# Optimization experiments

Hardware: AMD Instinct MI355X
Metric: run time of the kernel (lower is better)

## Reference

```python
import jax, jax.numpy as jnp
import numpy as np

D_MODEL = 1024
D_STATE = 64
D_CONV = 4
EXPAND = 2
HEADDIM = 64
D_INNER = EXPAND * D_MODEL            # 2048
NHEADS = D_INNER // HEADDIM           # 32
CONV_DIM = D_INNER + 2 * D_STATE      # 2176
D_IN_PROJ = 2 * D_INNER + 2 * D_STATE + NHEADS  # 4256
B, L = 2, 1024


def _mamba2(x, in_proj_w, conv_w, conv_b, dt_bias, A_log, D_param, rms_w, out_proj_w):
    b, l, _ = x.shape
    zxbcdt = x @ in_proj_w.T                                   # (b,l,4256)
    z, xBC, dt = jnp.split(zxbcdt, [D_INNER, D_INNER + CONV_DIM], axis=-1)
    dt = jax.nn.softplus(dt + dt_bias)                         # (b,l,h)
    # depthwise causal conv over sequence
    xBC = jax.lax.conv_general_dilated(
        xBC, conv_w, (1,), [(D_CONV - 1, 0)],
        dimension_numbers=("NLC", "LIO", "NLC"),
        feature_group_count=CONV_DIM) + conv_b
    xBC = jax.nn.silu(xBC)
    xs, Bmat, Cmat = jnp.split(xBC, [D_INNER, D_INNER + D_STATE], axis=-1)
    xh = xs.reshape(b, l, NHEADS, HEADDIM)
    A = -jnp.exp(A_log)                                        # (h,)
    dA = jnp.exp(dt * A)                                       # (b,l,h)

    def step(h, inp):
        dA_t, dt_t, B_t, C_t, x_t = inp                        # (b,h),(b,h),(b,n),(b,n),(b,h,p)
        h = h * dA_t[..., None, None] + (dt_t[..., None] * x_t)[..., None] * B_t[:, None, None, :]
        y_t = jnp.einsum("bhpn,bn->bhp", h, C_t)
        return h, y_t

    h0 = jnp.zeros((b, NHEADS, HEADDIM, D_STATE), x.dtype)
    inps = (dA.transpose(1, 0, 2), dt.transpose(1, 0, 2),
            Bmat.transpose(1, 0, 2), Cmat.transpose(1, 0, 2),
            xh.transpose(1, 0, 2, 3))
    _, ys = jax.lax.scan(step, h0, inps)                       # (l,b,h,p)
    y = ys.transpose(1, 0, 2, 3) + D_param[None, None, :, None] * xh
    y = y.reshape(b, l, D_INNER)
    # gated RMSNorm (norm after gating, as in mamba_ssm RMSNormGated)
    y = y * jax.nn.silu(z)
    y = y * jax.lax.rsqrt(jnp.mean(y * y, axis=-1, keepdims=True) + 1e-5) * rms_w
    return y @ out_proj_w.T


def setup_inputs() -> dict:
    key = jax.random.key(0)
    ks = jax.random.split(key, 16)
    s = 0.02

    def mamba_params(i):
        kk = jax.random.split(ks[i], 8)
        dt = jnp.exp(jax.random.uniform(kk[4], (NHEADS,)) * (np.log(0.1) - np.log(1e-3)) + np.log(1e-3))
        dt_bias = dt + jnp.log(-jnp.expm1(-dt))
        return dict(
            in_proj_w=jax.random.normal(kk[0], (D_IN_PROJ, D_MODEL)) * s,
            conv_w=jax.random.normal(kk[1], (D_CONV, 1, CONV_DIM)) * 0.2,
            conv_b=jnp.zeros((CONV_DIM,)),
            dt_bias=dt_bias,
            A_log=jnp.log(jax.random.uniform(kk[2], (NHEADS,), minval=1.0, maxval=16.0)),
            D=jnp.ones((NHEADS,)),
            rms_w=jnp.ones((D_INNER,)),
            out_proj_w=jax.random.normal(kk[3], (D_MODEL, D_INNER)) * s,
        )

    pf = mamba_params(1)
    pb = mamba_params(2)
    inp = {"x": jax.random.normal(ks[0], (B, L, D_MODEL))}
    for name, v in pf.items():
        inp["f_" + name] = v
    for name, v in pb.items():
        inp["b_" + name] = v
    inp["proj_w"] = jax.random.normal(ks[3], (D_MODEL, 2 * D_MODEL)) * s
    inp["proj_b"] = jnp.zeros((D_MODEL,))
    inp["ln_w"] = jnp.ones((D_MODEL,))
    inp["ln_b"] = jnp.zeros((D_MODEL,))
    return inp


def reference(x, f_in_proj_w, f_conv_w, f_conv_b, f_dt_bias, f_A_log, f_D, f_rms_w, f_out_proj_w,
              b_in_proj_w, b_conv_w, b_conv_b, b_dt_bias, b_A_log, b_D, b_rms_w, b_out_proj_w,
              proj_w, proj_b, ln_w, ln_b):
    out_fwd = _mamba2(x, f_in_proj_w, f_conv_w, f_conv_b, f_dt_bias, f_A_log, f_D, f_rms_w, f_out_proj_w)
    out_bwd = _mamba2(jnp.flip(x, 1), b_in_proj_w, b_conv_w, b_conv_b, b_dt_bias, b_A_log, b_D, b_rms_w, b_out_proj_w)
    out_bwd = jnp.flip(out_bwd, 1)
    combined = jnp.concatenate([out_fwd, out_bwd], axis=-1)
    h = x + combined @ proj_w.T + proj_b
    mu = jnp.mean(h, axis=-1, keepdims=True)
    var = jnp.mean((h - mu) ** 2, axis=-1, keepdims=True)
    return (h - mu) * jax.lax.rsqrt(var + 1e-5) * ln_w + ln_b
```

## Files before the change

### kernel.cpp

```cpp
#include <hip/hip_runtime.h>
#include <hip/hip_bf16.h>

#define DEV __device__ __forceinline__

typedef short bf16x8 __attribute__((ext_vector_type(8)));
typedef float f32x4 __attribute__((ext_vector_type(4)));

static constexpr int BATCH  = 2;
static constexpr int SEQ    = 1024;
static constexpr int DMODEL = 1024;
static constexpr int DINNER = 2048;
static constexpr int DSTATE = 64;
static constexpr int NH     = 32;
static constexpr int HD     = 64;
static constexpr int CONVD  = 2176;
static constexpr int DPROJ  = 4256;
static constexpr int MROWS  = BATCH * SEQ;
static constexpr int NCHUNK = 16;
static constexpr int QC     = 64;

static constexpr size_t OFF_ZX = 0;
static constexpr size_t OFF_XS = OFF_ZX + (size_t)2*MROWS*DPROJ*2;
static constexpr size_t OFF_BB = OFF_XS + (size_t)2*MROWS*DINNER*2;
static constexpr size_t OFF_CC = OFF_BB + (size_t)2*MROWS*DSTATE*4;
static constexpr size_t OFF_DT = OFF_CC + (size_t)2*MROWS*DSTATE*4;
static constexpr size_t OFF_DA = OFF_DT + (size_t)2*MROWS*NH*4;
static constexpr size_t OFF_DR = OFF_DA + (size_t)2*MROWS*NH*4;
static constexpr size_t OFF_CS = OFF_DR + (size_t)2*MROWS*NH*4;
static constexpr size_t OFF_DD = 0;
static constexpr size_t OFF_H  = OFF_DD + (size_t)MROWS*2*DMODEL;
static constexpr size_t OFF_WO = OFF_H  + (size_t)MROWS*DMODEL*4;
static constexpr size_t OFF_WP = OFF_WO + (size_t)2*DMODEL*DINNER*2;

DEV float b2f(ushort u) {
    union { unsigned int i; float f; } v;
    v.i = ((unsigned int)u) << 16;
    return v.f;
}
DEV ushort f2b(float f) {
    union { float f; unsigned int u; } v;
    v.f = f;
    unsigned int r = 0x7FFFu + ((v.u >> 16) & 1u);
    return (ushort)((v.u + r) >> 16);
}
DEV bf16x8 pack8(float4 a, float4 b) {
    bf16x8 r;
    r[0] = (short)f2b(a.x); r[1] = (short)f2b(a.y);
    r[2] = (short)f2b(a.z); r[3] = (short)f2b(a.w);
    r[4] = (short)f2b(b.x); r[5] = (short)f2b(b.y);
    r[6] = (short)f2b(b.z); r[7] = (short)f2b(b.w);
    return r;
}
DEV void gll16(const ushort* g, ushort* l) {
    __builtin_amdgcn_global_load_lds(
        (const __attribute__((address_space(1))) unsigned int*)g,
        (__attribute__((address_space(3))) unsigned int*)l, 16, 0, 0);
}

__global__ __launch_bounds__(256) void cvt3_k(
    const float* __restrict__ s0, const float* __restrict__ s1,
    const float* __restrict__ s2,
    ushort* __restrict__ d0, ushort* __restrict__ d1, ushort* __restrict__ d2,
    int b0, int b1)
{
    int blk = blockIdx.x;
    const float* s; ushort* d; size_t off;
    if (blk < b0)            { s = s0; d = d0; off = (size_t)blk * 1024; }
    else if (blk < b0 + b1)  { s = s1; d = d1; off = (size_t)(blk - b0) * 1024; }
    else                     { s = s2; d = d2; off = (size_t)(blk - b0 - b1) * 1024; }
    size_t i = off + threadIdx.x * 4;
    float4 f = *(const float4*)(s + i);
    ushort4 u;
    u.x = f2b(f.x); u.y = f2b(f.y); u.z = f2b(f.z); u.w = f2b(f.w);
    *(ushort4*)(d + i) = u;
}

template<int MODE, int BN>
__global__ __launch_bounds__(256) void gemm_k(
    const ushort* __restrict__ A, const ushort* __restrict__ W,
    size_t wstride, void* __restrict__ outp, const float* __restrict__ resid,
    const float* __restrict__ bias, float* __restrict__ dtraw,
    int N, int K)
{
    constexpr int BM = 128, BK = 64;
    constexpr int MT = (BN == 128) ? 4 : 2;
    constexpr int NBLB = (BN == 128) ? 4 : 2;
    __shared__ ushort As[BM * BK];
    __shared__ ushort Bs[BN * BK];
    const int tid = threadIdx.x;
    const int wave = tid >> 6, lane = tid & 63;
    const int quad = lane >> 4, l16 = lane & 15;
    const int bxu = (MODE == 0)
        ? (int)((blockIdx.x + 2 * blockIdx.y) % gridDim.x) : (int)blockIdx.x;
    const int bn = bxu * BN, bm = blockIdx.y * BM;
    const int dir = blockIdx.z;
    const ushort* Wd = W + (size_t)dir * wstride;
    const int wmoff = (BN == 128) ? (wave >> 1) * 64 : wave * 32;
    const int wnoff = (BN == 128) ? (wave & 1) * 64 : 0;

    const int scg = ((lane & 7) ^ ((lane >> 3) & 7)) * 8;
    const ushort* aga[4];
    ushort* ald[4];
    #pragma unroll
    for (int t = 0; t < 4; t++) {
        int li = wave * 4 + t;
        int r = li * 8 + (lane >> 3);
        int m = bm + r;
        size_t rowidx;
        if (MODE == 0) {
            int b = m >> 10, l = m & 1023;
            int ls = dir ? (1023 - l) : l;
            rowidx = (size_t)((b << 10) + ls);
        } else if (MODE == 1) {
            rowidx = (size_t)(dir * MROWS + m);
        } else {
            rowidx = (size_t)m;
        }
        aga[t] = A + rowidx * K + scg;
        ald[t] = &As[li * 512];
    }
    const ushort* bga[NBLB];
    ushort* bld[NBLB];
    #pragma unroll
    for (int t = 0; t < NBLB; t++) {
        int li = wave * NBLB + t;
        int n = bn + li * 8 + (lane >> 3);
        if (n >= N) n = N - 1;
        bga[t] = Wd + (size_t)n * K + scg;
        bld[t] = &Bs[li * 512];
    }

    f32x4 acc[MT][4] = {};

    for (int k0 = 0; k0 < K; k0 += BK) {
        #pragma unroll
        for (int t = 0; t < 4; t++) gll16(aga[t] + k0, ald[t]);
        #pragma unroll
        for (int t = 0; t < NBLB; t++) gll16(bga[t] + k0, bld[t]);
        __syncthreads();

        #pragma unroll
        for (int kt = 0; kt < 2; kt++) {
            const int rs = (((kt * 4 + quad) ^ (l16 & 7))) * 8;
            bf16x8 af[MT], bfr[4];
            #pragma unroll
            for (int mt = 0; mt < MT; mt++)
                af[mt] = *(const bf16x8*)&As[(wmoff + mt * 16 + l16) * BK + rs];
            #pragma unroll
            for (int nt = 0; nt < 4; nt++)
                bfr[nt] = *(const bf16x8*)&Bs[(wnoff + nt * 16 + l16) * BK + rs];
            #pragma unroll
            for (int mt = 0; mt < MT; mt++)
                #pragma unroll
                for (int nt = 0; nt < 4; nt++)
                    acc[mt][nt] = __builtin_amdgcn_mfma_f32_16x16x32_bf16(
                        af[mt], bfr[nt], acc[mt][nt], 0, 0, 0);
        }
        __syncthreads();
    }

    #pragma unroll
    for (int mt = 0; mt < MT; mt++) {
        #pragma unroll
        for (int nt = 0; nt < 4; nt++) {
            #pragma unroll
            for (int j = 0; j < 4; j++) {
                int row = bm + wmoff + mt * 16 + quad * 4 + j;
                int col = bn + wnoff + nt * 16 + l16;
                if (col >= N) continue;
                float v = acc[mt][nt][j];
                if (MODE == 0) {
                    ((ushort*)outp)[(size_t)(dir * MROWS + row) * DPROJ + col] = f2b(v);
                    if (col >= 4224)
                        dtraw[(size_t)(dir * MROWS + row) * NH + (col - 4224)] = v;
                } else if (MODE == 1) {
                    int mr = dir ? ((row & 1024) | (1023 - (row & 1023))) : row;
                    ((ushort*)outp)[(size_t)mr * (2 * DMODEL) + dir * DMODEL + col] = f2b(v);
                } else {
                    float r = resid[(size_t)row * DMODEL + col] + bias[col];
                    ((float*)outp)[(size_t)row * DMODEL + col] = v + r;
                }
            }
        }
    }
}

__global__ __launch_bounds__(256) void conv_k(
    const ushort* __restrict__ zx, const float* __restrict__ dtr,
    const float* __restrict__ cw0, const float* __restrict__ cb0,
    const float* __restrict__ cw1, const float* __restrict__ cb1,
    const float* __restrict__ dtb0, const float* __restrict__ al0,
    const float* __restrict__ dtb1, const float* __restrict__ al1,
    ushort* __restrict__ xs, float* __restrict__ Bq, float* __restrict__ Cq,
    float* __restrict__ dtq, float* __restrict__ ldq)
{
    int id = blockIdx.x;
    int dir = id >> 11;
    int m = id & 2047;
    int l = m & 1023;
    const float* cw = dir ? cw1 : cw0;
    const float* cb = dir ? cb1 : cb0;
    int tid = threadIdx.x;

    for (int c = tid * 4; c < CONVD; c += 1024) {
        float4 cbv = *(const float4*)&cb[c];
        float acc[4] = { cbv.x, cbv.y, cbv.z, cbv.w };
        #pragma unroll
        for (int t = 0; t < 4; t++) {
            int ls = l - 3 + t;
            if (ls >= 0) {
                float4 wv = *(const float4*)&cw[t * CONVD + c];
                ushort4 xv = *(const ushort4*)&zx[(size_t)(id - l + ls) * DPROJ + 2048 + c];
                acc[0] += wv.x * b2f(xv.x);
                acc[1] += wv.y * b2f(xv.y);
                acc[2] += wv.z * b2f(xv.z);
                acc[3] += wv.w * b2f(xv.w);
            }
        }
        float v[4];
        #pragma unroll
        for (int i = 0; i < 4; i++) v[i] = acc[i] / (1.f + expf(-acc[i]));
        if (c < DINNER) {
            ushort4 u;
            u.x = f2b(v[0]); u.y = f2b(v[1]); u.z = f2b(v[2]); u.w = f2b(v[3]);
            *(ushort4*)&xs[(size_t)id * DINNER + c] = u;
        } else if (c < DINNER + DSTATE) {
            *(float4*)&Bq[(size_t)id * DSTATE + (c - DINNER)] =
                make_float4(v[0], v[1], v[2], v[3]);
        } else {
            *(float4*)&Cq[(size_t)id * DSTATE + (c - DINNER - DSTATE)] =
                make_float4(v[0], v[1], v[2], v[3]);
        }
    }
    if (tid < NH) {
        const float* dtb = dir ? dtb1 : dtb0;
        const float* al  = dir ? al1 : al0;
        float raw = dtr[(size_t)id * NH + tid] + dtb[tid];
        float dt = raw > 20.f ? raw : log1pf(expf(raw));
        float ldA = -expf(al[tid]) * dt;
        int dirb = id >> 10;
        dtq[(size_t)(dirb * NH + tid) * SEQ + l] = dt;
        ldq[(size_t)(dirb * NH + tid) * SEQ + l] = ldA;
    }
}

__global__ __launch_bounds__(256) void states_k(
    const float* __restrict__ Bq, const float* __restrict__ dtT,
    const float* __restrict__ ldT, const ushort* __restrict__ xsq,
    ushort* __restrict__ cs)
{
    int id = blockIdx.x;
    int h = id & 31;
    int c = blockIdx.y;
    int tid = threadIdx.x;
    int wave = tid >> 6, lane = tid & 63;
    int quad = lane >> 4;
    int base = (id >> 5) << 10;
    int l0 = c * QC;

    __shared__ float wsh[QC];
    __shared__ ushort Xw[64][80];
    __shared__ ushort Bt[64][72];

    if (tid < 64) {
        float ld = ldT[(size_t)id * SEQ + l0 + tid];
        #pragma unroll
        for (int st = 1; st < 64; st <<= 1) {
            float o = __shfl_up(ld, st);
            if (tid >= st) ld += o;
        }
        float tot = __shfl(ld, 63);
        wsh[tid] = dtT[(size_t)id * SEQ + l0 + tid] * expf(tot - ld);
    }
    __syncthreads();

    {
        int j = tid >> 2, p0 = (tid & 3) * 16;
        float wj = wsh[j];
        const ushort* xrow = xsq + (size_t)(base + l0 + j) * DINNER + h * HD + p0;
        #pragma unroll
        for (int q = 0; q < 4; q++) {
            ushort4 xv = *(const ushort4*)(xrow + q * 4);
            Xw[p0 + q * 4 + 0][j] = f2b(b2f(xv.x) * wj);
            Xw[p0 + q * 4 + 1][j] = f2b(b2f(xv.y) * wj);
            Xw[p0 + q * 4 + 2][j] = f2b(b2f(xv.z) * wj);
            Xw[p0 + q * 4 + 3][j] = f2b(b2f(xv.w) * wj);
        }
        int j2 = lane, ng = wave * 16;
        const float* brow = Bq + (size_t)(base + l0 + j2) * DSTATE + ng;
        #pragma unroll
        for (int q = 0; q < 4; q++) {
            float4 f = *(const float4*)(brow + q * 4);
            Bt[ng + q * 4 + 0][j2] = f2b(f.x);
            Bt[ng + q * 4 + 1][j2] = f2b(f.y);
            Bt[ng + q * 4 + 2][j2] = f2b(f.z);
            Bt[ng + q * 4 + 3][j2] = f2b(f.w);
        }
    }
    __syncthreads();

    f32x4 acc[4] = {};
    #pragma unroll
    for (int kt = 0; kt < 2; kt++) {
        int k = kt * 32 + quad * 8;
        bf16x8 af = *(const bf16x8*)&Xw[wave * 16 + (lane & 15)][k];
        #pragma unroll
        for (int ni = 0; ni < 4; ni++) {
            bf16x8 bf = *(const bf16x8*)&Bt[ni * 16 + (lane & 15)][k];
            acc[ni] = __builtin_amdgcn_mfma_f32_16x16x32_bf16(af, bf, acc[ni], 0, 0, 0);
        }
    }

    ushort* out = cs + ((size_t)id * NCHUNK + c) * HD * DSTATE;
    #pragma unroll
    for (int ni = 0; ni < 4; ni++) {
        #pragma unroll
        for (int j = 0; j < 4; j++) {
            int p = wave * 16 + quad * 4 + j;
            int n = ni * 16 + (lane & 15);
            out[(size_t)p * DSTATE + n] = f2b(acc[ni][j]);
        }
    }
}

__global__ __launch_bounds__(256) void stitch_k(
    const float* __restrict__ ldT, ushort* __restrict__ cs)
{
    int id = blockIdx.x;
    int tid = threadIdx.x;
    __shared__ float red[256];
    __shared__ float dec[NCHUNK];

    float4 d4 = *(const float4*)(ldT + (size_t)id * SEQ + tid * 4);
    red[tid] = d4.x + d4.y + d4.z + d4.w;
    __syncthreads();
    if (tid < NCHUNK) {
        float s = 0.f;
        #pragma unroll
        for (int i = 0; i < 16; i++) s += red[tid * 16 + i];
        dec[tid] = expf(s);
    }
    __syncthreads();

    int p = tid >> 2, n0 = (tid & 3) * 16;
    ushort* ptr = cs + (size_t)id * NCHUNK * HD * DSTATE + p * DSTATE + n0;

    float st[16];
    #pragma unroll
    for (int i = 0; i < 16; i++) st[i] = 0.f;

    for (int c = 0; c < NCHUNK; c++) {
        ushort* row = ptr + (size_t)c * HD * DSTATE;
        float tmp[16];
        #pragma unroll
        for (int i = 0; i < 16; i++) tmp[i] = b2f(row[i]);
        #pragma unroll
        for (int i = 0; i < 16; i++) row[i] = f2b(st[i]);
        float d = dec[c];
        #pragma unroll
        for (int i = 0; i < 16; i++) st[i] = fmaf(d, st[i], tmp[i]);
    }
}

__global__ __launch_bounds__(256) void ssd_k(
    const float* __restrict__ Bq, const float* __restrict__ Cq,
    const float* __restrict__ dtT, const float* __restrict__ ldT,
    const ushort* __restrict__ xsq, const ushort* __restrict__ cs,
    const float* __restrict__ D0, const float* __restrict__ D1,
    ushort* __restrict__ yout)
{
    int id = blockIdx.x;
    int dir = id >> 6, h = id & 31;
    int c = blockIdx.y;
    int tid = threadIdx.x;
    int wave = tid >> 6, lane = tid & 63;
    int quad = lane >> 4;
    int base = (id >> 5) << 10;
    int l0 = c * QC;

    __shared__ float cum[QC], dts[QC];
    __shared__ ushort Ms[64][72];
    __shared__ ushort Xb[64][80];

    {
        int j = tid >> 2, p0 = (tid & 3) * 16;
        const ushort* xrow = xsq + (size_t)(base + l0 + j) * DINNER + h * HD + p0;
        #pragma unroll
        for (int q = 0; q < 4; q++) {
            ushort4 xv = *(const ushort4*)(xrow + q * 4);
            Xb[p0 + q * 4 + 0][j] = xv.x;
            Xb[p0 + q * 4 + 1][j] = xv.y;
            Xb[p0 + q * 4 + 2][j] = xv.z;
            Xb[p0 + q * 4 + 3][j] = xv.w;
        }
    }
    if (tid < 64) {
        float ld = ldT[(size_t)id * SEQ + l0 + tid];
        #pragma unroll
        for (int st = 1; st < 64; st <<= 1) {
            float o = __shfl_up(ld, st);
            if (tid >= st) ld += o;
        }
        cum[tid] = ld;
        dts[tid] = dtT[(size_t)id * SEQ + l0 + tid];
    }

    f32x4 sacc[4] = {};
    #pragma unroll
    for (int kt = 0; kt < 2; kt++) {
        int k = kt * 32 + quad * 8;
        const float* cp = Cq + (size_t)(base + l0 + wave * 16 + (lane & 15)) * DSTATE + k;
        bf16x8 af = pack8(*(const float4*)cp, *(const float4*)(cp + 4));
        #pragma unroll
        for (int ni = 0; ni < 4; ni++) {
            const float* bp = Bq + (size_t)(base + l0 + ni * 16 + (lane & 15)) * DSTATE + k;
            bf16x8 bf = pack8(*(const float4*)bp, *(const float4*)(bp + 4));
            sacc[ni] = __builtin_amdgcn_mfma_f32_16x16x32_bf16(af, bf, sacc[ni], 0, 0, 0);
        }
    }
    __syncthreads();

    #pragma unroll
    for (int ni = 0; ni < 4; ni++) {
        int j = ni * 16 + (lane & 15);
        float cj = cum[j], dj = dts[j];
        #pragma unroll
        for (int r = 0; r < 4; r++) {
            int l = wave * 16 + quad * 4 + r;
            float v = 0.f;
            if (l >= j) v = expf(cum[l] - cj) * dj * sacc[ni][r];
            Ms[l][j] = f2b(v);
        }
    }
    __syncthreads();

    f32x4 acc[4] = {};
    #pragma unroll
    for (int kt = 0; kt < 2; kt++) {
        int k = kt * 32 + quad * 8;
        bf16x8 af = *(const bf16x8*)&Ms[wave * 16 + (lane & 15)][k];
        #pragma unroll
        for (int ni = 0; ni < 4; ni++) {
            bf16x8 bf = *(const bf16x8*)&Xb[ni * 16 + (lane & 15)][k];
            acc[ni] = __builtin_amdgcn_mfma_f32_16x16x32_bf16(af, bf, acc[ni], 0, 0, 0);
        }
    }
    const ushort* Hrow = cs + ((size_t)id * NCHUNK + c) * HD * DSTATE;
    {
        float cl = expf(cum[wave * 16 + (lane & 15)]);
        #pragma unroll
        for (int kt = 0; kt < 2; kt++) {
            int k = kt * 32 + quad * 8;
            const float* cp = Cq + (size_t)(base + l0 + wave * 16 + (lane & 15)) * DSTATE + k;
            float4 c0 = *(const float4*)cp;
            float4 c1 = *(const float4*)(cp + 4);
            float4 s0 = {c0.x * cl, c0.y * cl, c0.z * cl, c0.w * cl};
            float4 s1 = {c1.x * cl, c1.y * cl, c1.z * cl, c1.w * cl};
            bf16x8 af = pack8(s0, s1);
            #pragma unroll
            for (int ni = 0; ni < 4; ni++) {
                bf16x8 bf = *(const bf16x8*)(Hrow + (size_t)(ni * 16 + (lane & 15)) * DSTATE + k);
                acc[ni] = __builtin_amdgcn_mfma_f32_16x16x32_bf16(af, bf, acc[ni], 0, 0, 0);
            }
        }
    }

    float Dv = (dir ? D1 : D0)[h];
    int lb = wave * 16 + quad * 4;
    #pragma unroll
    for (int ni = 0; ni < 4; ni++) {
        int p = ni * 16 + (lane & 15);
        ushort4 x4 = *(const ushort4*)&Xb[p][lb];
        float xv[4] = { b2f(x4.x), b2f(x4.y), b2f(x4.z), b2f(x4.w) };
        #pragma unroll
        for (int r = 0; r < 4; r++) {
            int l = lb + r;
            yout[(size_t)(base + l0 + l) * DPROJ + 2048 + h * HD + p] =
                f2b(acc[ni][r] + Dv * xv[r]);
        }
    }
}

__global__ __launch_bounds__(256) void grms_k(
    const ushort* __restrict__ zx,
    const float* __restrict__ rw0, const float* __restrict__ rw1,
    ushort* __restrict__ yn)
{
    int id = blockIdx.x;
    int dir = id >> 11;
    const float* rw = dir ? rw1 : rw0;
    int tid = threadIdx.x;
    int c0 = tid * 8;
    ushort zv[8], yv[8];
    *(uint4*)zv = *(const uint4*)&zx[(size_t)id * DPROJ + c0];
    *(uint4*)yv = *(const uint4*)&zx[(size_t)id * DPROJ + 2048 + c0];
    float g[8];
    float ss = 0.f;
    #pragma unroll
    for (int i = 0; i < 8; i++) {
        float z = b2f(zv[i]);
        float v = b2f(yv[i]) * (z / (1.f + expf(-z)));
        g[i] = v;
        ss += v * v;
    }
    for (int o = 32; o; o >>= 1) ss += __shfl_down(ss, o);
    __shared__ float t4[4];
    if ((tid & 63) == 0) t4[tid >> 6] = ss;
    __syncthreads();
    ss = t4[0] + t4[1] + t4[2] + t4[3];
    float sc = rsqrtf(ss * (1.f / DINNER) + 1e-5f);
    ushort u[8];
    #pragma unroll
    for (int i = 0; i < 8; i++) u[i] = f2b(g[i] * sc * rw[c0 + i]);
    *(uint4*)&yn[(size_t)id * DINNER + c0] = *(uint4*)u;
}

__global__ __launch_bounds__(256) void ln_k(
    const float* __restrict__ h, const float* __restrict__ lw,
    const float* __restrict__ lb, float* __restrict__ out)
{
    int m = blockIdx.x;
    int tid = threadIdx.x;
    int c = tid * 4;
    float4 v = *(const float4*)&h[(size_t)m * DMODEL + c];
    float s  = v.x + v.y + v.z + v.w;
    float s2 = v.x * v.x + v.y * v.y + v.z * v.z + v.w * v.w;
    for (int o = 32; o; o >>= 1) { s += __shfl_down(s, o); s2 += __shfl_down(s2, o); }
    __shared__ float ts[4], ts2[4];
    if ((tid & 63) == 0) { ts[tid >> 6] = s; ts2[tid >> 6] = s2; }
    __syncthreads();
    s  = ts[0] + ts[1] + ts[2] + ts[3];
    s2 = ts2[0] + ts2[1] + ts2[2] + ts2[3];
    float mu  = s * (1.f / DMODEL);
    float var = s2 * (1.f / DMODEL) - mu * mu;
    float sc  = rsqrtf(var + 1e-5f);
    float4 w4 = *(const float4*)&lw[c];
    float4 b4 = *(const float4*)&lb[c];
    float4 o4;
    o4.x = (v.x - mu) * sc * w4.x + b4.x;
    o4.y = (v.y - mu) * sc * w4.y + b4.y;
    o4.z = (v.z - mu) * sc * w4.z + b4.z;
    o4.w = (v.w - mu) * sc * w4.w + b4.w;
    *(float4*)&out[(size_t)m * DMODEL + c] = o4;
}

extern "C" void kernel_launch(void* const* d_in, const int* in_sizes, int n_in,
                              void* d_out, int out_size, void* d_ws, size_t ws_size,
                              hipStream_t stream)
{
    const float* x     = (const float*)d_in[0];
    const float* f_inw = (const float*)d_in[1];
    const float* f_cw  = (const float*)d_in[2];
    const float* f_cb  = (const float*)d_in[3];
    const float* f_dtb = (const float*)d_in[4];
    const float* f_al  = (const float*)d_in[5];
    const float* f_Dp  = (const float*)d_in[6];
    const float* f_rw  = (const float*)d_in[7];
    const float* f_ow  = (const float*)d_in[8];
    const float* b_inw = (const float*)d_in[9];
    const float* b_cw  = (const float*)d_in[10];
    const float* b_cb  = (const float*)d_in[11];
    const float* b_dtb = (const float*)d_in[12];
    const float* b_al  = (const float*)d_in[13];
    const float* b_Dp  = (const float*)d_in[14];
    const float* b_rw  = (const float*)d_in[15];
    const float* b_ow  = (const float*)d_in[16];
    const float* projw = (const float*)d_in[17];
    const float* projb = (const float*)d_in[18];
    const float* lnw   = (const float*)d_in[19];
    const float* lnb   = (const float*)d_in[20];

    char* ws = (char*)d_ws;
    ushort* zx  = (ushort*)(ws + OFF_ZX);
    ushort* xs  = (ushort*)(ws + OFF_XS);
    float*  Bq  = (float*)(ws + OFF_BB);
    float*  Cq  = (float*)(ws + OFF_CC);
    float*  dtq = (float*)(ws + OFF_DT);
    float*  ldq = (float*)(ws + OFF_DA);
    float*  dtr = (float*)(ws + OFF_DR);
    ushort* wbf = (ushort*)(ws + OFF_CS);
    ushort* cs  = (ushort*)(ws + OFF_CS);
    ushort* xbf = (ushort*)(ws + OFF_XS);
    ushort* yn  = (ushort*)(ws + OFF_XS);
    ushort* dd  = (ushort*)(ws + OFF_DD);
    float*  hb  = (float*)(ws + OFF_H);
    ushort* wo  = (ushort*)(ws + OFF_WO);
    ushort* wp  = (ushort*)(ws + OFF_WP);

    cvt3_k<<<dim3(2 * DPROJ + MROWS), 256, 0, stream>>>(
        f_inw, b_inw, x, wbf, wbf + (size_t)DPROJ * DMODEL, xbf, DPROJ, DPROJ);

    gemm_k<0, 128><<<dim3((DPROJ + 127) / 128, MROWS / 128, 2), 256, 0, stream>>>(
        xbf, wbf, (size_t)DPROJ * DMODEL, (void*)zx, nullptr, nullptr, dtr,
        DPROJ, DMODEL);

    conv_k<<<dim3(2 * MROWS), 256, 0, stream>>>(
        zx, dtr, f_cw, f_cb, b_cw, b_cb, f_dtb, f_al, b_dtb, b_al,
        xs, Bq, Cq, dtq, ldq);

    states_k<<<dim3(128, NCHUNK), 256, 0, stream>>>(Bq, dtq, ldq, xs, cs);
    stitch_k<<<dim3(128), 256, 0, stream>>>(ldq, cs);
    ssd_k<<<dim3(128, NCHUNK), 256, 0, stream>>>(
        Bq, Cq, dtq, ldq, xs, cs, f_Dp, b_Dp, zx);

    grms_k<<<dim3(2 * MROWS), 256, 0, stream>>>(zx, f_rw, b_rw, yn);

    cvt3_k<<<dim3(3 * MROWS), 256, 0, stream>>>(
        f_ow, b_ow, projw, wo, wo + (size_t)DMODEL * DINNER, wp, MROWS, MROWS);

    gemm_k<1, 64><<<dim3(DMODEL / 64, MROWS / 128, 2), 256, 0, stream>>>(
        yn, wo, (size_t)DMODEL * DINNER, (void*)dd, nullptr, nullptr, nullptr,
        DMODEL, DINNER);

    gemm_k<2, 64><<<dim3(DMODEL / 64, MROWS / 128, 1), 256, 0, stream>>>(
        dd, wp, 0, (void*)hb, x, projb, nullptr, DMODEL, DINNER);

    ln_k<<<dim3(MROWS), 256, 0, stream>>>(hb, lnw, lnb, (float*)d_out);
}
```

Baseline: 362.4 us.

## Fuse gated RMSNorm with weight conversion and deepen K tile for output GEMMs

Merges the gated RMSNorm kernel and the out_proj/proj_w fp32-to-bf16 conversion into one launch, so the two independent workloads share a grid and one launch is removed. The GEMM kernel gains a BK template parameter with generalized swizzled loading, and the two output GEMMs use BK=128 to halve the number of K-loop iterations and barriers. The converted weights are relocated into the CS workspace region so they no longer overlap the output buffers. Larger BK doubles shared memory per block, which may lower occupancy.

```diff
diff --git a/kernel.cpp b/kernel.cpp
--- a/kernel.cpp
+++ b/kernel.cpp
@@ -27,10 +27,10 @@
 static constexpr size_t OFF_DA = OFF_DT + (size_t)2*MROWS*NH*4;
 static constexpr size_t OFF_DR = OFF_DA + (size_t)2*MROWS*NH*4;
 static constexpr size_t OFF_CS = OFF_DR + (size_t)2*MROWS*NH*4;
+static constexpr size_t OFF_WO = OFF_CS;
+static constexpr size_t OFF_WP = OFF_CS + (size_t)2*DMODEL*DINNER*2;
 static constexpr size_t OFF_DD = 0;
 static constexpr size_t OFF_H  = OFF_DD + (size_t)MROWS*2*DMODEL;
-static constexpr size_t OFF_WO = OFF_H  + (size_t)MROWS*DMODEL*4;
-static constexpr size_t OFF_WP = OFF_WO + (size_t)2*DMODEL*DINNER*2;
 
 DEV float b2f(ushort u) {
     union { unsigned int i; float f; } v;
@@ -75,16 +75,19 @@
     *(ushort4*)(d + i) = u;
 }
 
-template<int MODE, int BN>
+template<int MODE, int BN, int BK>
 __global__ __launch_bounds__(256) void gemm_k(
     const ushort* __restrict__ A, const ushort* __restrict__ W,
     size_t wstride, void* __restrict__ outp, const float* __restrict__ resid,
     const float* __restrict__ bias, float* __restrict__ dtraw,
     int N, int K)
 {
-    constexpr int BM = 128, BK = 64;
+    constexpr int BM = 128;
     constexpr int MT = (BN == 128) ? 4 : 2;
-    constexpr int NBLB = (BN == 128) ? 4 : 2;
+    constexpr int NSL = BK / 8;
+    constexpr int RPG = 64 / NSL;
+    constexpr int NAG = BM / RPG / 4;
+    constexpr int NBG = BN / RPG / 4;
     __shared__ ushort As[BM * BK];
     __shared__ ushort Bs[BN * BK];
     const int tid = threadIdx.x;
@@ -98,14 +101,14 @@
     const int wmoff = (BN == 128) ? (wave >> 1) * 64 : wave * 32;
     const int wnoff = (BN == 128) ? (wave & 1) * 64 : 0;
 
-    const int scg = ((lane & 7) ^ ((lane >> 3) & 7)) * 8;
-    const ushort* aga[4];
-    ushort* ald[4];
-    #pragma unroll
-    for (int t = 0; t < 4; t++) {
-        int li = wave * 4 + t;
-        int r = li * 8 + (lane >> 3);
-        int m = bm + r;
+    const int lrow = lane / NSL, lslot = lane % NSL;
+    const ushort* aga[NAG];
+    ushort* ald[NAG];
+    #pragma unroll
+    for (int t = 0; t < NAG; t++) {
+        int li = wave * NAG + t;
+        int absr = li * RPG + lrow;
+        int m = bm + absr;
         size_t rowidx;
         if (MODE == 0) {
             int b = m >> 10, l = m & 1023;
@@ -116,17 +119,18 @@
         } else {
             rowidx = (size_t)m;
         }
-        aga[t] = A + rowidx * K + scg;
+        aga[t] = A + rowidx * K + (lslot ^ (absr % NSL)) * 8;
         ald[t] = &As[li * 512];
     }
-    const ushort* bga[NBLB];
-    ushort* bld[NBLB];
-    #pragma unroll
-    for (int t = 0; t < NBLB; t++) {
-        int li = wave * NBLB + t;
-        int n = bn + li * 8 + (lane >> 3);
+    const ushort* bga[NBG];
+    ushort* bld[NBG];
+    #pragma unroll
+    for (int t = 0; t < NBG; t++) {
+        int li = wave * NBG + t;
+        int absr = li * RPG + lrow;
+        int n = bn + absr;
         if (n >= N) n = N - 1;
-        bga[t] = Wd + (size_t)n * K + scg;
+        bga[t] = Wd + (size_t)n * K + (lslot ^ (absr % NSL)) * 8;
         bld[t] = &Bs[li * 512];
     }
 
@@ -134,14 +138,14 @@
 
     for (int k0 = 0; k0 < K; k0 += BK) {
         #pragma unroll
-        for (int t = 0; t < 4; t++) gll16(aga[t] + k0, ald[t]);
-        #pragma unroll
-        for (int t = 0; t < NBLB; t++) gll16(bga[t] + k0, bld[t]);
+        for (int t = 0; t < NAG; t++) gll16(aga[t] + k0, ald[t]);
+        #pragma unroll
+        for (int t = 0; t < NBG; t++) gll16(bga[t] + k0, bld[t]);
         __syncthreads();
 
         #pragma unroll
-        for (int kt = 0; kt < 2; kt++) {
-            const int rs = (((kt * 4 + quad) ^ (l16 & 7))) * 8;
+        for (int kt = 0; kt < BK / 32; kt++) {
+            const int rs = (((kt * 4 + quad) ^ (l16 % NSL))) * 8;
             bf16x8 af[MT], bfr[4];
             #pragma unroll
             for (int mt = 0; mt < MT; mt++)
@@ -481,15 +485,32 @@
     }
 }
 
-__global__ __launch_bounds__(256) void grms_k(
+__global__ __launch_bounds__(256) void grms_cvt_k(
     const ushort* __restrict__ zx,
     const float* __restrict__ rw0, const float* __restrict__ rw1,
-    ushort* __restrict__ yn)
-{
-    int id = blockIdx.x;
+    ushort* __restrict__ yn,
+    const float* __restrict__ fow, const float* __restrict__ bow,
+    const float* __restrict__ pw,
+    ushort* __restrict__ wo, ushort* __restrict__ wp)
+{
+    int blk = blockIdx.x;
+    int tid = threadIdx.x;
+    if (blk >= 4096) {
+        int b = blk - 4096;
+        const float* s; ushort* d; size_t off;
+        if (b < 2048)      { s = fow; d = wo;                           off = (size_t)b * 1024; }
+        else if (b < 4096) { s = bow; d = wo + (size_t)DMODEL * DINNER; off = (size_t)(b - 2048) * 1024; }
+        else               { s = pw;  d = wp;                           off = (size_t)(b - 4096) * 1024; }
+        size_t i = off + tid * 4;
+        float4 f = *(const float4*)(s + i);
+        ushort4 u;
+        u.x = f2b(f.x); u.y = f2b(f.y); u.z = f2b(f.z); u.w = f2b(f.w);
+        *(ushort4*)(d + i) = u;
+        return;
+    }
+    int id = blk;
     int dir = id >> 11;
     const float* rw = dir ? rw1 : rw0;
-    int tid = threadIdx.x;
     int c0 = tid * 8;
     ushort zv[8], yv[8];
     *(uint4*)zv = *(const uint4*)&zx[(size_t)id * DPROJ + c0];
@@ -590,7 +611,7 @@
     cvt3_k<<<dim3(2 * DPROJ + MROWS), 256, 0, stream>>>(
         f_inw, b_inw, x, wbf, wbf + (size_t)DPROJ * DMODEL, xbf, DPROJ, DPROJ);
 
-    gemm_k<0, 128><<<dim3((DPROJ + 127) / 128, MROWS / 128, 2), 256, 0, stream>>>(
+    gemm_k<0, 128, 64><<<dim3((DPROJ + 127) / 128, MROWS / 128, 2), 256, 0, stream>>>(
         xbf, wbf, (size_t)DPROJ * DMODEL, (void*)zx, nullptr, nullptr, dtr,
         DPROJ, DMODEL);
 
@@ -603,16 +624,14 @@
     ssd_k<<<dim3(128, NCHUNK), 256, 0, stream>>>(
         Bq, Cq, dtq, ldq, xs, cs, f_Dp, b_Dp, zx);
 
-    grms_k<<<dim3(2 * MROWS), 256, 0, stream>>>(zx, f_rw, b_rw, yn);
-
-    cvt3_k<<<dim3(3 * MROWS), 256, 0, stream>>>(
-        f_ow, b_ow, projw, wo, wo + (size_t)DMODEL * DINNER, wp, MROWS, MROWS);
-
-    gemm_k<1, 64><<<dim3(DMODEL / 64, MROWS / 128, 2), 256, 0, stream>>>(
+    grms_cvt_k<<<dim3(4096 + 3 * MROWS), 256, 0, stream>>>(
+        zx, f_rw, b_rw, yn, f_ow, b_ow, projw, wo, wp);
+
+    gemm_k<1, 64, 128><<<dim3(DMODEL / 64, MROWS / 128, 2), 256, 0, stream>>>(
         yn, wo, (size_t)DMODEL * DINNER, (void*)dd, nullptr, nullptr, nullptr,
         DMODEL, DINNER);
 
-    gemm_k<2, 64><<<dim3(DMODEL / 64, MROWS / 128, 1), 256, 0, stream>>>(
+    gemm_k<2, 64, 128><<<dim3(DMODEL / 64, MROWS / 128, 1), 256, 0, stream>>>(
         dd, wp, 0, (void*)hb, x, projb, nullptr, DMODEL, DINNER);
 
     ln_k<<<dim3(MROWS), 256, 0, stream>>>(hb, lnw, lnb, (float*)d_out);
```

Result: faster. 350.6 us (-3.2%).
